# Optimization experiments

Hardware: AMD Instinct MI355X
Metric: run time of the kernel (lower is better)

The kernel has to match this reference:

```python
import jax, jax.numpy as jnp
import numpy as np

N = 200000          # real (non-pad) faces
P = 8192            # pad entries
PAD = N + P         # padded table size
C_IN = 128
C_OUT = 128


def setup_inputs() -> dict:
    key = jax.random.key(0)
    ks = jax.random.split(key, 6)
    x = jax.random.normal(ks[0], (N, C_IN), jnp.float32)
    # column 0 = the face itself (a real, non-pad index); columns 1..8 = neighbors
    col0 = jnp.arange(N, dtype=jnp.int64)[:, None]
    nbrs = jax.random.randint(ks[1], (N, 8), 0, PAD, dtype=jnp.int64)
    face_neighborhood = jnp.concatenate([col0, nbrs], axis=1)
    face_is_pad = jnp.arange(PAD) >= N  # last P rows are padding
    s = 1.0 / np.sqrt(C_IN).astype(np.float32)
    in_proj_w = jax.random.normal(ks[2], (3 * C_IN, C_IN), jnp.float32) * s
    in_proj_b = jnp.zeros((3 * C_IN,), jnp.float32)
    out_proj_w = jax.random.normal(ks[3], (C_IN, C_IN), jnp.float32) * s
    out_proj_b = jnp.zeros((C_IN,), jnp.float32)
    conv_w = jax.random.normal(ks[4], (C_OUT, C_IN, 1, 2), jnp.float32) * (1.0 / np.sqrt(2.0 * C_IN).astype(np.float32))
    conv_b = jnp.zeros((C_OUT,), jnp.float32)
    return {
        "x": x,
        "face_neighborhood": face_neighborhood,
        "face_is_pad": face_is_pad,
        "pad_size": PAD,
        "in_proj_w": in_proj_w,
        "in_proj_b": in_proj_b,
        "out_proj_w": out_proj_w,
        "out_proj_b": out_proj_b,
        "conv_w": conv_w,
        "conv_b": conv_b,
    }


def reference(x, face_neighborhood, face_is_pad, pad_size,
              in_proj_w, in_proj_b, out_proj_w, out_proj_b, conv_w, conv_b):
    C = x.shape[1]
    H = max(1, C // 32)
    Dh = C // H
    # scatter real features into the padded table (padded_x[~face_is_pad] = x)
    nonpad_idx = jnp.nonzero(~face_is_pad, size=x.shape[0])[0]
    padded_x = jnp.zeros((pad_size, C), x.dtype).at[nonpad_idx].set(x)
    f = padded_x[face_neighborhood]              # [N, 9, C] 9-way gather
    center = f[:, 0]                             # [N, C] query feature
    kv = f[:, 1:]                                # [N, 8, C]
    # torch MultiheadAttention: packed in_proj then per-head scaled dot-product
    q = (center @ in_proj_w[:C].T + in_proj_b[:C]).reshape(-1, 1, H, Dh).transpose(0, 2, 1, 3)       # [N,H,1,Dh]
    k = (kv @ in_proj_w[C:2 * C].T + in_proj_b[C:2 * C]).reshape(-1, 8, H, Dh).transpose(0, 2, 1, 3)  # [N,H,8,Dh]
    v = (kv @ in_proj_w[2 * C:].T + in_proj_b[2 * C:]).reshape(-1, 8, H, Dh).transpose(0, 2, 1, 3)    # [N,H,8,Dh]
    scale = 1.0 / jnp.sqrt(jnp.asarray(Dh, q.dtype))
    scores = jnp.einsum('nhqd,nhkd->nhqk', q, k) * scale  # [N,H,1,8]
    pad_mask = face_is_pad[face_neighborhood[:, 1:]][:, None, None, :]  # [N,1,1,8]
    scores = jnp.where(pad_mask, -jnp.inf, scores)
    attn = jax.nn.softmax(scores, axis=-1)
    o = jnp.einsum('nhqk,nhkd->nhqd', attn, v)            # [N,H,1,Dh]
    o = o.transpose(0, 2, 1, 3).reshape(-1, C)            # [N,C] (q_len==1)
    h = o @ out_proj_w.T + out_proj_b                     # [N,C]
    # Conv2d(C_in, C_out, (1,2)) over [N, C, 1, 2] == linear fuse of center & h
    out = center @ conv_w[:, :, 0, 0].T + h @ conv_w[:, :, 0, 1].T + conv_b  # [N, C_out]
    return out
```

## Files before the change

kernel.cpp:

```cpp
#include <hip/hip_runtime.h>

typedef __bf16 bfrag __attribute__((ext_vector_type(8)));
typedef float f32x4 __attribute__((ext_vector_type(4)));

__device__ __forceinline__ unsigned short f2bf(float f) {
  unsigned u = __float_as_uint(f);
  u = (u + 0x7fffu + ((u >> 16) & 1u)) >> 16;
  return (unsigned short)u;
}
__device__ __forceinline__ float bflo(unsigned u) { return __uint_as_float(u << 16); }
__device__ __forceinline__ float bfhi(unsigned u) { return __uint_as_float(u & 0xffff0000u); }

__global__ void k_prep(const float* __restrict__ in_proj_w,
                       const float* __restrict__ conv_w,
                       const float* __restrict__ out_proj_w,
                       const float* __restrict__ out_proj_b,
                       const float* __restrict__ conv_b,
                       unsigned short* __restrict__ WcatF,
                       unsigned short* __restrict__ W2F,
                       float* __restrict__ cvec) {
  int b = blockIdx.x, t = threadIdx.x;
  if (b < 384) {
    unsigned short v = f2bf(in_proj_w[b * 128 + t]);
    int cb = b >> 7, r7 = b & 127;
    int cB = r7 >> 4, mr = r7 & 15;
    int ks = t >> 5, quad = (t >> 3) & 3, j = t & 7;
    WcatF[(((cb * 8 + cB) * 4 + ks) << 9) + (quad * 16 + mr) * 8 + j] = v;
  } else {
    int c = b - 384;
    int cB = c >> 4, mr = c & 15;
    float s = 0.f;
    for (int k = 0; k < 128; ++k)
      s += conv_w[(c * 128 + k) * 2 + 1] * out_proj_w[k * 128 + t];
    {
      int kc = t >> 6, ks2 = (t >> 5) & 1, quad = (t >> 3) & 3, j = t & 7;
      W2F[(((cB * 4 + kc) * 2 + ks2) << 9) + (quad * 16 + mr) * 8 + j] = f2bf(s);
    }
    {
      int K = 128 + t;
      int kc = K >> 6, ks2 = (K >> 5) & 1, quad = (K >> 3) & 3, j = K & 7;
      W2F[(((cB * 4 + kc) * 2 + ks2) << 9) + (quad * 16 + mr) * 8 + j] =
          f2bf(conv_w[(c * 128 + t) * 2]);
    }
    if (t == 0) {
      float cs = conv_b[c];
      for (int k = 0; k < 128; ++k)
        cs += conv_w[(c * 128 + k) * 2 + 1] * out_proj_b[k];
      cvec[c] = cs;
    }
  }
}

__global__ __launch_bounds__(256, 4) void k_gemm_qkv(
    const float* __restrict__ x, const unsigned short* __restrict__ WcatF,
    const float* __restrict__ in_proj_b, unsigned short* __restrict__ Qb,
    unsigned short* __restrict__ KVb, int M) {
  __shared__ unsigned short se[4][32 * 72];
  const int m0 = blockIdx.x * 128;
  const int t = threadIdx.x;
  const int w = t >> 6, lane = t & 63, quad = lane >> 4, mr = lane & 15;
  unsigned short* sew = se[w];

  bfrag af[4][2];
#pragma unroll
  for (int ks = 0; ks < 4; ++ks)
#pragma unroll
    for (int r = 0; r < 2; ++r) {
      int row = m0 + w * 32 + r * 16 + mr;
      union { unsigned short s[8]; bfrag f; } u;
      if (row < M) {
        const float4* p =
            reinterpret_cast<const float4*>(&x[(size_t)row * 128 + ks * 32 + quad * 8]);
        float4 v0 = p[0], v1 = p[1];
        u.s[0] = f2bf(v0.x); u.s[1] = f2bf(v0.y); u.s[2] = f2bf(v0.z); u.s[3] = f2bf(v0.w);
        u.s[4] = f2bf(v1.x); u.s[5] = f2bf(v1.y); u.s[6] = f2bf(v1.z); u.s[7] = f2bf(v1.w);
      } else {
#pragma unroll
        for (int i = 0; i < 8; ++i) u.s[i] = 0;
      }
      af[ks][r] = u.f;
    }

#pragma unroll
  for (int cb = 0; cb < 3; ++cb) {
    unsigned short* dst = (cb == 0) ? Qb : KVb;
    const int ldst = (cb == 0) ? 128 : 256;
    const int cb_off = (cb == 2) ? 128 : 0;
#pragma unroll
    for (int half = 0; half < 2; ++half) {
      f32x4 acc[2][4];
#pragma unroll
      for (int r = 0; r < 2; ++r)
#pragma unroll
        for (int c = 0; c < 4; ++c) acc[r][c] = (f32x4){0.f, 0.f, 0.f, 0.f};
#pragma unroll
      for (int ks = 0; ks < 4; ++ks)
#pragma unroll
        for (int c = 0; c < 4; ++c) {
          union { uint4 v; bfrag f; } u;
          u.v = *reinterpret_cast<const uint4*>(
              &WcatF[(((cb * 8 + half * 4 + c) * 4 + ks) << 9) + lane * 8]);
          acc[0][c] = __builtin_amdgcn_mfma_f32_16x16x32_bf16(af[ks][0], u.f, acc[0][c], 0, 0, 0);
          acc[1][c] = __builtin_amdgcn_mfma_f32_16x16x32_bf16(af[ks][1], u.f, acc[1][c], 0, 0, 0);
        }
      const float* bias = in_proj_b + cb * 128 + half * 64;
#pragma unroll
      for (int r = 0; r < 2; ++r)
#pragma unroll
        for (int c = 0; c < 4; ++c) {
          float bv = bias[c * 16 + mr];
#pragma unroll
          for (int g = 0; g < 4; ++g)
            sew[(r * 16 + quad * 4 + g) * 72 + c * 16 + mr] = f2bf(acc[r][c][g] + bv);
        }
#pragma unroll
      for (int i = 0; i < 4; ++i) {
        int ch = i * 64 + lane;
        int row = ch >> 3, cp = ch & 7;
        int grow = m0 + w * 32 + row;
        if (grow < M) {
          uint4 v = *reinterpret_cast<const uint4*>(&sew[row * 72 + cp * 8]);
          *reinterpret_cast<uint4*>(
              &dst[(size_t)grow * ldst + cb_off + half * 64 + cp * 8]) = v;
        }
      }
    }
  }
}

__global__ __launch_bounds__(256) void k_attn(
    const unsigned short* __restrict__ Qb, const unsigned short* __restrict__ KVb,
    const int* __restrict__ fn, unsigned short* __restrict__ Ob, int M) {
  int w = threadIdx.x >> 6, lane = threadIdx.x & 63;
  int n = blockIdx.x * 4 + w;
  if (n >= M) return;
  const float scale = 0.17677669529663687f;
  const int l5 = lane & 31;
  uint2 qp = *reinterpret_cast<const uint2*>(&Qb[(size_t)n * 128 + 4 * l5]);
  float q0 = bflo(qp.x), q1 = bfhi(qp.x), q2 = bflo(qp.y), q3 = bfhi(qp.y);
  int idx[8];
#pragma unroll
  for (int j = 0; j < 8; ++j) idx[j] = fn[n * 9 + 1 + j];
  float o0 = 0.f, o1 = 0.f, o2 = 0.f, o3 = 0.f, sum = 0.f;
#pragma unroll
  for (int j = 0; j < 8; ++j) {
    bool valid = idx[j] < M;
    int id = valid ? idx[j] : 0;
    uint2 kv = *reinterpret_cast<const uint2*>(&KVb[(size_t)id * 256 + 4 * lane]);
    float a0 = bflo(kv.x), a1 = bfhi(kv.x), a2 = bflo(kv.y), a3 = bfhi(kv.y);
    float p = q0 * a0 + q1 * a1 + q2 * a2 + q3 * a3;
    p += __shfl_xor(p, 1);
    p += __shfl_xor(p, 2);
    p += __shfl_xor(p, 4);
    float pu = __shfl_xor(p, 32);
    float sf = (lane >= 32) ? pu : p;
    float s = valid ? sf * scale : -1e30f;
    float e = __expf(s);
    sum += e;
    o0 += e * a0; o1 += e * a1; o2 += e * a2; o3 += e * a3;
  }
  float inv = 1.f / sum;
  if (lane >= 32) {
    union { unsigned short s[4]; uint2 u; } p;
    p.s[0] = f2bf(o0 * inv); p.s[1] = f2bf(o1 * inv);
    p.s[2] = f2bf(o2 * inv); p.s[3] = f2bf(o3 * inv);
    *reinterpret_cast<uint2*>(&Ob[(size_t)n * 128 + 4 * l5]) = p.u;
  }
}

__global__ __launch_bounds__(256, 4) void k_gemm_out(
    const unsigned short* __restrict__ Ob, const float* __restrict__ x,
    const unsigned short* __restrict__ W2F, const float* __restrict__ cvec,
    float* __restrict__ out, int M) {
  __shared__ float sf[4][32 * 36];
  const int m0 = blockIdx.x * 128;
  const int t = threadIdx.x;
  const int w = t >> 6, lane = t & 63, quad = lane >> 4, mr = lane & 15;
  float* sfw = sf[w];

  f32x4 acc[2][8];
#pragma unroll
  for (int r = 0; r < 2; ++r)
#pragma unroll
    for (int c = 0; c < 8; ++c) acc[r][c] = (f32x4){0.f, 0.f, 0.f, 0.f};

#pragma unroll
  for (int kc = 0; kc < 4; ++kc) {
    bfrag af[2][2];
#pragma unroll
    for (int ks2 = 0; ks2 < 2; ++ks2)
#pragma unroll
      for (int r = 0; r < 2; ++r) {
        int row = m0 + w * 32 + r * 16 + mr;
        if (kc < 2) {
          union { uint4 v; bfrag f; } u;
          u.v = make_uint4(0u, 0u, 0u, 0u);
          if (row < M)
            u.v = *reinterpret_cast<const uint4*>(
                &Ob[(size_t)row * 128 + kc * 64 + ks2 * 32 + quad * 8]);
          af[ks2][r] = u.f;
        } else {
          union { unsigned short s[8]; bfrag f; } u;
          if (row < M) {
            const float4* p = reinterpret_cast<const float4*>(
                &x[(size_t)row * 128 + (kc - 2) * 64 + ks2 * 32 + quad * 8]);
            float4 v0 = p[0], v1 = p[1];
            u.s[0] = f2bf(v0.x); u.s[1] = f2bf(v0.y); u.s[2] = f2bf(v0.z); u.s[3] = f2bf(v0.w);
            u.s[4] = f2bf(v1.x); u.s[5] = f2bf(v1.y); u.s[6] = f2bf(v1.z); u.s[7] = f2bf(v1.w);
          } else {
#pragma unroll
            for (int i = 0; i < 8; ++i) u.s[i] = 0;
          }
          af[ks2][r] = u.f;
        }
      }
#pragma unroll
    for (int ks2 = 0; ks2 < 2; ++ks2)
#pragma unroll
      for (int c = 0; c < 8; ++c) {
        union { uint4 v; bfrag f; } u;
        u.v = *reinterpret_cast<const uint4*>(
            &W2F[(((c * 4 + kc) * 2 + ks2) << 9) + lane * 8]);
        acc[0][c] = __builtin_amdgcn_mfma_f32_16x16x32_bf16(af[ks2][0], u.f, acc[0][c], 0, 0, 0);
        acc[1][c] = __builtin_amdgcn_mfma_f32_16x16x32_bf16(af[ks2][1], u.f, acc[1][c], 0, 0, 0);
      }
  }
#pragma unroll
  for (int p = 0; p < 4; ++p) {
#pragma unroll
    for (int cc = 0; cc < 2; ++cc) {
      int c = p * 2 + cc;
      float cv = cvec[c * 16 + mr];
#pragma unroll
      for (int r = 0; r < 2; ++r)
#pragma unroll
        for (int g = 0; g < 4; ++g)
          sfw[(r * 16 + quad * 4 + g) * 36 + cc * 16 + mr] = acc[r][c][g] + cv;
    }
#pragma unroll
    for (int i = 0; i < 4; ++i) {
      int ch = i * 64 + lane;
      int row = ch >> 3, c4 = ch & 7;
      int grow = m0 + w * 32 + row;
      if (grow < M) {
        float4 v = *reinterpret_cast<const float4*>(&sfw[row * 36 + c4 * 4]);
        *reinterpret_cast<float4*>(&out[(size_t)grow * 128 + p * 32 + c4 * 4]) = v;
      }
    }
  }
}

extern "C" void kernel_launch(void* const* d_in, const int* in_sizes, int n_in,
                              void* d_out, int out_size, void* d_ws, size_t ws_size,
                              hipStream_t stream) {
  const float* x          = (const float*)d_in[0];
  const int*   fn         = (const int*)d_in[1];
  const float* in_proj_w  = (const float*)d_in[4];
  const float* in_proj_b  = (const float*)d_in[5];
  const float* out_proj_w = (const float*)d_in[6];
  const float* out_proj_b = (const float*)d_in[7];
  const float* conv_w     = (const float*)d_in[8];
  const float* conv_b     = (const float*)d_in[9];
  const int M = in_sizes[0] / 128;

  unsigned short* KVb = (unsigned short*)d_out;
  char* ws = (char*)d_ws;
  unsigned short* Qb    = (unsigned short*)ws;
  unsigned short* Ob    = (unsigned short*)(ws + (size_t)M * 128 * 2);
  unsigned short* WcatF = (unsigned short*)(ws + (size_t)M * 128 * 4);
  unsigned short* W2F   = WcatF + 384 * 128;
  float*          cvec  = (float*)(W2F + 128 * 256);

  const int mt = (M + 127) / 128;
  k_prep<<<dim3(512), dim3(128), 0, stream>>>(in_proj_w, conv_w, out_proj_w,
                                              out_proj_b, conv_b, WcatF, W2F, cvec);
  k_gemm_qkv<<<dim3(mt), dim3(256), 0, stream>>>(x, WcatF, in_proj_b, Qb, KVb, M);
  k_attn<<<dim3((M + 3) / 4), dim3(256), 0, stream>>>(Qb, KVb, fn, Ob, M);
  k_gemm_out<<<dim3(mt), dim3(256), 0, stream>>>(Ob, x, W2F, cvec, (float*)d_out, M);
}
```

Before: 441.6 us.

## Fuse neighborhood attention with output projection GEMM in one kernel

Adds a kernel where each wave computes attention for 32 rows, stores the bf16 outputs in shared memory, and feeds them directly into the MFMA output/conv GEMM. This removes the global write and read of the intermediate attention output and one kernel launch. KV moves to the workspace, so the fused path runs only when the workspace is large enough; otherwise the old path runs. The trade-off is less parallelism in the attention phase, since rows are processed sequentially per wave.

```diff
diff --git a/kernel.cpp b/kernel.cpp
--- a/kernel.cpp
+++ b/kernel.cpp
@@ -128,6 +128,129 @@
   }
 }
 
+__global__ __launch_bounds__(256, 4) void k_fused(
+    const unsigned short* __restrict__ Qb, const unsigned short* __restrict__ KVb,
+    const int* __restrict__ fn, const float* __restrict__ x,
+    const unsigned short* __restrict__ W2F, const float* __restrict__ cvec,
+    float* __restrict__ out, int M) {
+  __shared__ unsigned short Os[4][32 * 136];
+  const int m0 = blockIdx.x * 128;
+  const int t = threadIdx.x;
+  const int w = t >> 6, lane = t & 63, quad = lane >> 4, mr = lane & 15;
+  unsigned short* Ow = Os[w];
+
+  {
+    const float scale = 0.17677669529663687f;
+    const int l5 = lane & 31;
+    for (int ri = 0; ri < 32; ++ri) {
+      const int n = m0 + w * 32 + ri;
+      if (n >= M) break;
+      uint2 qp = *reinterpret_cast<const uint2*>(&Qb[(size_t)n * 128 + 4 * l5]);
+      float q0 = bflo(qp.x), q1 = bfhi(qp.x), q2 = bflo(qp.y), q3 = bfhi(qp.y);
+      int idx[8];
+#pragma unroll
+      for (int j = 0; j < 8; ++j) idx[j] = fn[n * 9 + 1 + j];
+      float o0 = 0.f, o1 = 0.f, o2 = 0.f, o3 = 0.f, sum = 0.f;
+#pragma unroll
+      for (int j = 0; j < 8; ++j) {
+        bool valid = idx[j] < M;
+        int id = valid ? idx[j] : 0;
+        uint2 kv = *reinterpret_cast<const uint2*>(&KVb[(size_t)id * 256 + 4 * lane]);
+        float a0 = bflo(kv.x), a1 = bfhi(kv.x), a2 = bflo(kv.y), a3 = bfhi(kv.y);
+        float p = q0 * a0 + q1 * a1 + q2 * a2 + q3 * a3;
+        p += __shfl_xor(p, 1);
+        p += __shfl_xor(p, 2);
+        p += __shfl_xor(p, 4);
+        float pu = __shfl_xor(p, 32);
+        float sv = (lane >= 32) ? pu : p;
+        float s = valid ? sv * scale : -1e30f;
+        float e = __expf(s);
+        sum += e;
+        o0 += e * a0; o1 += e * a1; o2 += e * a2; o3 += e * a3;
+      }
+      float inv = 1.f / sum;
+      if (lane >= 32) {
+        union { unsigned short s[4]; uint2 u; } pk;
+        pk.s[0] = f2bf(o0 * inv); pk.s[1] = f2bf(o1 * inv);
+        pk.s[2] = f2bf(o2 * inv); pk.s[3] = f2bf(o3 * inv);
+        *reinterpret_cast<uint2*>(&Ow[ri * 136 + 4 * l5]) = pk.u;
+      }
+    }
+  }
+
+  f32x4 acc[2][8];
+#pragma unroll
+  for (int r = 0; r < 2; ++r)
+#pragma unroll
+    for (int c = 0; c < 8; ++c) acc[r][c] = (f32x4){0.f, 0.f, 0.f, 0.f};
+
+#pragma unroll
+  for (int kc = 0; kc < 4; ++kc) {
+    bfrag af[2][2];
+#pragma unroll
+    for (int ks2 = 0; ks2 < 2; ++ks2)
+#pragma unroll
+      for (int r = 0; r < 2; ++r) {
+        if (kc < 2) {
+          union { uint4 v; bfrag f; } u;
+          u.v = *reinterpret_cast<const uint4*>(
+              &Ow[(r * 16 + mr) * 136 + kc * 64 + ks2 * 32 + quad * 8]);
+          af[ks2][r] = u.f;
+        } else {
+          int row = m0 + w * 32 + r * 16 + mr;
+          union { unsigned short s[8]; bfrag f; } u;
+          if (row < M) {
+            const float4* p = reinterpret_cast<const float4*>(
+                &x[(size_t)row * 128 + (kc - 2) * 64 + ks2 * 32 + quad * 8]);
+            float4 v0 = p[0], v1 = p[1];
+            u.s[0] = f2bf(v0.x); u.s[1] = f2bf(v0.y); u.s[2] = f2bf(v0.z); u.s[3] = f2bf(v0.w);
+            u.s[4] = f2bf(v1.x); u.s[5] = f2bf(v1.y); u.s[6] = f2bf(v1.z); u.s[7] = f2bf(v1.w);
+          } else {
+#pragma unroll
+            for (int i = 0; i < 8; ++i) u.s[i] = 0;
+          }
+          af[ks2][r] = u.f;
+        }
+      }
+#pragma unroll
+    for (int ks2 = 0; ks2 < 2; ++ks2)
+#pragma unroll
+      for (int c = 0; c < 8; ++c) {
+        union { uint4 v; bfrag f; } u;
+        u.v = *reinterpret_cast<const uint4*>(
+            &W2F[(((c * 4 + kc) * 2 + ks2) << 9) + lane * 8]);
+        acc[0][c] = __builtin_amdgcn_mfma_f32_16x16x32_bf16(af[ks2][0], u.f, acc[0][c], 0, 0, 0);
+        acc[1][c] = __builtin_amdgcn_mfma_f32_16x16x32_bf16(af[ks2][1], u.f, acc[1][c], 0, 0, 0);
+      }
+  }
+
+  __syncthreads();
+  float* sfw = reinterpret_cast<float*>(Ow);
+#pragma unroll
+  for (int p = 0; p < 4; ++p) {
+#pragma unroll
+    for (int cc = 0; cc < 2; ++cc) {
+      int c = p * 2 + cc;
+      float cv = cvec[c * 16 + mr];
+#pragma unroll
+      for (int r = 0; r < 2; ++r)
+#pragma unroll
+        for (int g = 0; g < 4; ++g)
+          sfw[(r * 16 + quad * 4 + g) * 36 + cc * 16 + mr] = acc[r][c][g] + cv;
+    }
+#pragma unroll
+    for (int i = 0; i < 4; ++i) {
+      int ch = i * 64 + lane;
+      int row = ch >> 3, c4 = ch & 7;
+      int grow = m0 + w * 32 + row;
+      if (grow < M) {
+        float4 v = *reinterpret_cast<const float4*>(&sfw[row * 36 + c4 * 4]);
+        *reinterpret_cast<float4*>(&out[(size_t)grow * 128 + p * 32 + c4 * 4]) = v;
+      }
+    }
+  }
+}
+
 __global__ __launch_bounds__(256) void k_attn(
     const unsigned short* __restrict__ Qb, const unsigned short* __restrict__ KVb,
     const int* __restrict__ fn, unsigned short* __restrict__ Ob, int M) {
@@ -262,19 +385,37 @@
   const float* conv_w     = (const float*)d_in[8];
   const float* conv_b     = (const float*)d_in[9];
   const int M = in_sizes[0] / 128;
-
-  unsigned short* KVb = (unsigned short*)d_out;
+  const int mt = (M + 127) / 128;
   char* ws = (char*)d_ws;
-  unsigned short* Qb    = (unsigned short*)ws;
-  unsigned short* Ob    = (unsigned short*)(ws + (size_t)M * 128 * 2);
-  unsigned short* WcatF = (unsigned short*)(ws + (size_t)M * 128 * 4);
-  unsigned short* W2F   = WcatF + 384 * 128;
-  float*          cvec  = (float*)(W2F + 128 * 256);
-
-  const int mt = (M + 127) / 128;
-  k_prep<<<dim3(512), dim3(128), 0, stream>>>(in_proj_w, conv_w, out_proj_w,
-                                              out_proj_b, conv_b, WcatF, W2F, cvec);
-  k_gemm_qkv<<<dim3(mt), dim3(256), 0, stream>>>(x, WcatF, in_proj_b, Qb, KVb, M);
-  k_attn<<<dim3((M + 3) / 4), dim3(256), 0, stream>>>(Qb, KVb, fn, Ob, M);
-  k_gemm_out<<<dim3(mt), dim3(256), 0, stream>>>(Ob, x, W2F, cvec, (float*)d_out, M);
-}
+
+  const size_t qbytes  = (size_t)M * 128 * 2;
+  const size_t kvbytes = (size_t)M * 256 * 2;
+  const size_t wbytes  = (size_t)(384 * 128 + 128 * 256) * 2 + 512;
+
+  if (ws_size >= qbytes + kvbytes + wbytes) {
+    unsigned short* Qb    = (unsigned short*)ws;
+    unsigned short* KVb   = (unsigned short*)(ws + qbytes);
+    unsigned short* WcatF = (unsigned short*)(ws + qbytes + kvbytes);
+    unsigned short* W2F   = WcatF + 384 * 128;
+    float*          cvec  = (float*)(W2F + 128 * 256);
+
+    k_prep<<<dim3(512), dim3(128), 0, stream>>>(in_proj_w, conv_w, out_proj_w,
+                                                out_proj_b, conv_b, WcatF, W2F, cvec);
+    k_gemm_qkv<<<dim3(mt), dim3(256), 0, stream>>>(x, WcatF, in_proj_b, Qb, KVb, M);
+    k_fused<<<dim3(mt), dim3(256), 0, stream>>>(Qb, KVb, fn, x, W2F, cvec,
+                                                (float*)d_out, M);
+  } else {
+    unsigned short* KVb   = (unsigned short*)d_out;
+    unsigned short* Qb    = (unsigned short*)ws;
+    unsigned short* Ob    = (unsigned short*)(ws + (size_t)M * 128 * 2);
+    unsigned short* WcatF = (unsigned short*)(ws + (size_t)M * 128 * 4);
+    unsigned short* W2F   = WcatF + 384 * 128;
+    float*          cvec  = (float*)(W2F + 128 * 256);
+
+    k_prep<<<dim3(512), dim3(128), 0, stream>>>(in_proj_w, conv_w, out_proj_w,
+                                                out_proj_b, conv_b, WcatF, W2F, cvec);
+    k_gemm_qkv<<<dim3(mt), dim3(256), 0, stream>>>(x, WcatF, in_proj_b, Qb, KVb, M);
+    k_attn<<<dim3((M + 3) / 4), dim3(256), 0, stream>>>(Qb, KVb, fn, Ob, M);
+    k_gemm_out<<<dim3(mt), dim3(256), 0, stream>>>(Ob, x, W2F, cvec, (float*)d_out, M);
+  }
+}
```

Result: no change. 448.2 us (+1.5%).
